# Performance work log

Measured on AMD Instinct MI355X. Metric: run time of the kernel, lower is better.

The kernel has to match this reference:

```python
import jax, jax.numpy as jnp
import numpy as np

B, P, F = 128, 4096, 32
K, D = 8, 64
ITERS = 2
EPS_ATTN = 1e-8
EPS_LN = 1e-5
SCALE = D ** -0.5


def _layernorm(x, g, b):
    mu = jnp.mean(x, axis=-1, keepdims=True)
    var = jnp.mean((x - mu) ** 2, axis=-1, keepdims=True)
    return (x - mu) * jax.lax.rsqrt(var + EPS_LN) * g + b


def setup_inputs() -> dict:
    key = jax.random.key(0)
    ks = jax.random.split(key, 16)
    s = lambda fan_in: 1.0 / np.sqrt(fan_in)
    inp = {
        "x": jax.random.normal(ks[0], (B, P, F), dtype=jnp.float32),
        "noise": jax.random.normal(ks[1], (B, K, D), dtype=jnp.float32),
        "slots_mu": jax.random.normal(ks[2], (1, 1, D), dtype=jnp.float32),
        "slots_sigma": jnp.ones((1, 1, D), dtype=jnp.float32) * 0.1,
        # torch Linear weights: [out, in]
        "Wq": jax.random.uniform(ks[3], (D, D), jnp.float32, -s(D), s(D)),
        "Wk": jax.random.uniform(ks[4], (D, F), jnp.float32, -s(F), s(F)),
        "Wv": jax.random.uniform(ks[5], (D, F), jnp.float32, -s(F), s(F)),
        # GRUCell params: weight_ih/[3D,D], weight_hh/[3D,D], biases [3D]
        "W_ih": jax.random.uniform(ks[6], (3 * D, D), jnp.float32, -s(D), s(D)),
        "W_hh": jax.random.uniform(ks[7], (3 * D, D), jnp.float32, -s(D), s(D)),
        "b_ih": jax.random.uniform(ks[8], (3 * D,), jnp.float32, -s(D), s(D)),
        "b_hh": jax.random.uniform(ks[9], (3 * D,), jnp.float32, -s(D), s(D)),
        "ln_in_g": jnp.ones((F,), jnp.float32),
        "ln_in_b": jnp.zeros((F,), jnp.float32),
        "ln_slots_g": jnp.ones((D,), jnp.float32),
        "ln_slots_b": jnp.zeros((D,), jnp.float32),
        "ff_ln_g": jnp.ones((D,), jnp.float32),
        "ff_ln_b": jnp.zeros((D,), jnp.float32),
        "ff_W1": jax.random.uniform(ks[10], (2 * D, D), jnp.float32, -s(D), s(D)),
        "ff_b1": jax.random.uniform(ks[11], (2 * D,), jnp.float32, -s(D), s(D)),
        "ff_W2": jax.random.uniform(ks[12], (D, 2 * D), jnp.float32, -s(2 * D), s(2 * D)),
        "ff_b2": jax.random.uniform(ks[13], (D,), jnp.float32, -s(2 * D), s(2 * D)),
    }
    return inp


def _gru_cell(x, h, W_ih, W_hh, b_ih, b_hh):
    # x, h: [N, D]
    gi = x @ W_ih.T + b_ih  # [N, 3D]
    gh = h @ W_hh.T + b_hh
    i_r, i_z, i_n = jnp.split(gi, 3, axis=-1)
    h_r, h_z, h_n = jnp.split(gh, 3, axis=-1)
    r = jax.nn.sigmoid(i_r + h_r)
    z = jax.nn.sigmoid(i_z + h_z)
    n = jnp.tanh(i_n + r * h_n)
    return (1.0 - z) * n + z * h


def reference(x, noise, slots_mu, slots_sigma, Wq, Wk, Wv, W_ih, W_hh, b_ih, b_hh,
              ln_in_g, ln_in_b, ln_slots_g, ln_slots_b,
              ff_ln_g, ff_ln_b, ff_W1, ff_b1, ff_W2, ff_b2):
    x_norm = _layernorm(x, ln_in_g, ln_in_b)          # [B,P,F]
    k = x_norm @ Wk.T                                  # [B,P,D]
    v = x_norm @ Wv.T                                  # [B,P,D]
    slots = slots_mu + jnp.abs(slots_sigma) * noise    # [B,K,D]
    last_attn = None
    for _ in range(ITERS):
        slots_prev = slots
        q = _layernorm(slots, ln_slots_g, ln_slots_b) @ Wq.T  # [B,K,D]
        dots = jnp.einsum('bkd,bpd->bkp', q, k) * SCALE       # [B,K,P]
        attn = jax.nn.softmax(dots, axis=1) + EPS_ATTN        # softmax over slots
        attn = attn / jnp.sum(attn, axis=-1, keepdims=True)   # normalize over pixels
        last_attn = attn
        updates = jnp.einsum('bkp,bpd->bkd', attn, v)         # [B,K,D]
        h = _gru_cell(updates.reshape(-1, D), slots_prev.reshape(-1, D),
                      W_ih, W_hh, b_ih, b_hh).reshape(x.shape[0], K, D)
        ff_in = _layernorm(h, ff_ln_g, ff_ln_b)
        ff_out = jax.nn.relu(ff_in @ ff_W1.T + ff_b1) @ ff_W2.T + ff_b2
        slots = h + ff_out
    return slots, last_attn
```

## Files before the change

kernel.cpp:

```cpp
#include <hip/hip_runtime.h>
#include <hip/hip_bf16.h>
#include <stdint.h>

#define Bb 128
#define Pp 4096
#define Ff 32
#define Kk 8
#define Dd 64
#define ROUNDS 2
#define NSLICE 32

constexpr float EPS_ATTN_ = 1e-8f;
constexpr float EPS_LN_   = 1e-5f;
constexpr float SCALE_    = 0.125f;

typedef __attribute__((ext_vector_type(8))) short short8;
typedef __attribute__((ext_vector_type(4))) float floatx4;

__device__ __forceinline__ unsigned short f2bf(float f) {
  union { float f; unsigned u; } c; c.f = f;
  unsigned u = c.u + 0x7fffu + ((c.u >> 16) & 1u);
  return (unsigned short)(u >> 16);
}
__device__ __forceinline__ float bf2f(unsigned h) {
  union { float f; unsigned u; } c; c.u = h << 16;
  return c.f;
}
__device__ __forceinline__ unsigned pkbf(float a, float b) {
  __hip_bfloat162 h2 = __float22bfloat162_rn(make_float2(a, b));
  union { __hip_bfloat162 h; unsigned u; } c; c.h = h2;
  return c.u;
}
__device__ __forceinline__ float wsum(float v) {
  v += __shfl_xor(v, 1, 64);  v += __shfl_xor(v, 2, 64);
  v += __shfl_xor(v, 4, 64);  v += __shfl_xor(v, 8, 64);
  v += __shfl_xor(v, 16, 64); v += __shfl_xor(v, 32, 64);
  return v;
}

template <bool ITER2>
__global__ __launch_bounds__(256, 4) void fattn_kernel(
    const float* __restrict__ x, const unsigned short* __restrict__ qt_bf,
    const float* __restrict__ lg, const float* __restrict__ lb,
    const float* __restrict__ noise, const float* __restrict__ smu,
    const float* __restrict__ ssig, const float* __restrict__ Wq,
    const float* __restrict__ Wk, const float* __restrict__ lsg,
    const float* __restrict__ lsb,
    float* __restrict__ acc_tp, float* __restrict__ Ssp,
    unsigned short* __restrict__ attn_bf) {
  const int b    = blockIdx.x;
  const int yb   = blockIdx.y;
  const int w    = threadIdx.x >> 6;
  const int lane = threadIdx.x & 63;
  const int m    = lane & 15;
  const int quad = lane >> 4;
  const int c    = (lane & 7) * 4;
  __shared__ __align__(16) char smem[40960];
  unsigned short* xb  = (unsigned short*)smem;
  unsigned short* xbT = (unsigned short*)(smem + 20480);
  unsigned short (*A_lds)[8][64] = (unsigned short (*)[8][64])(smem + 36864);

  const float4* xg4 =
      (const float4*)x + ((size_t)b * Pp + (size_t)yb * (ROUNDS * 256)) * 8;
  float4 st[8];
  #pragma unroll
  for (int i = 0; i < 8; ++i)
    st[i] = xg4[w * 512 + i * 64 + lane];

  const float4 lgv = *(const float4*)&lg[c];
  const float4 lbv = *(const float4*)&lb[c];

  short8 aq;
  if (!ITER2) {
    float* wq  = (float*)smem;
    float* wk  = (float*)(smem + 16640);
    float* lnv = (float*)(smem + 25088);
    unsigned short* qtb = (unsigned short*)(smem + 27136);
    {
      const float4* g4 = (const float4*)Wq;
      #pragma unroll
      for (int i = 0; i < 4; ++i) {
        int f4i = threadIdx.x + i * 256;
        float4 v = g4[f4i];
        int fi = f4i * 4, row = fi >> 6, col = fi & 63;
        float* dst = &wq[row * 65 + col];
        dst[0] = v.x; dst[1] = v.y; dst[2] = v.z; dst[3] = v.w;
      }
      const float4* gk = (const float4*)Wk;
      #pragma unroll
      for (int i = 0; i < 2; ++i) {
        int f4i = threadIdx.x + i * 256;
        float4 v = gk[f4i];
        int fi = f4i * 4, row = fi >> 5, col = fi & 31;
        float* dst = &wk[row * 33 + col];
        dst[0] = v.x; dst[1] = v.y; dst[2] = v.z; dst[3] = v.w;
      }
    }
    const int j = lane;
    #pragma unroll
    for (int kk0 = 0; kk0 < 2; ++kk0) {
      const int kk = w + kk0 * 4;
      float s0 = smu[j] + fabsf(ssig[j]) * noise[((size_t)b * Kk + kk) * Dd + j];
      float mu  = wsum(s0) * (1.f / 64.f);
      float dc  = s0 - mu;
      float var = wsum(dc * dc) * (1.f / 64.f);
      lnv[kk * 64 + j] = dc * rsqrtf(var + EPS_LN_) * lsg[j] + lsb[j];
    }
    __syncthreads();
    float qa = 0.f, qb = 0.f;
    #pragma unroll 8
    for (int d = 0; d < Dd; ++d) {
      float wv = wq[j * 65 + d];
      qa = fmaf(wv, lnv[w * 64 + d],       qa);
      qb = fmaf(wv, lnv[(w + 4) * 64 + d], qb);
    }
    __syncthreads();
    lnv[w * 64 + j]       = qa * SCALE_;
    lnv[(w + 4) * 64 + j] = qb * SCALE_;
    __syncthreads();
    {
      const int kq = threadIdx.x >> 5, fq = threadIdx.x & 31;
      float qt = 0.f;
      #pragma unroll 8
      for (int d = 0; d < Dd; ++d) qt = fmaf(lnv[kq * 64 + d], wk[d * 33 + fq], qt);
      qtb[kq * 32 + fq]       = f2bf(qt);
      qtb[(kq + 8) * 32 + fq] = 0;
    }
    __syncthreads();
    aq = *(const short8*)&qtb[m * 32 + quad * 8];
    __syncthreads();
  } else {
    aq = *(const short8*)(qt_bf + ((size_t)b * 16 + m) * Ff + quad * 8);
  }

  float Ss0 = 0.f, Ss1 = 0.f, Ss2 = 0.f, Ss3 = 0.f;
  floatx4 Cg0 = {0.f,0.f,0.f,0.f}, Cg1 = {0.f,0.f,0.f,0.f};

  #pragma unroll 1
  for (int rr = 0; rr < ROUNDS; ++rr) {
    #pragma unroll
    for (int i = 0; i < 8; ++i) {
      float4 v = st[i];
      if (rr + 1 < ROUNDS)
        st[i] = xg4[(rr + 1) * 2048 + w * 512 + i * 64 + lane];
      float s = (v.x + v.y) + (v.z + v.w);
      s += __shfl_xor(s, 1, 64);
      s += __shfl_xor(s, 2, 64);
      s += __shfl_xor(s, 4, 64);
      const float mu = s * (1.f / 32.f);
      const float d0 = v.x - mu, d1 = v.y - mu, d2 = v.z - mu, d3 = v.w - mu;
      float q = fmaf(d0, d0, fmaf(d1, d1, fmaf(d2, d2, d3 * d3)));
      q += __shfl_xor(q, 1, 64);
      q += __shfl_xor(q, 2, 64);
      q += __shfl_xor(q, 4, 64);
      const float rn = rsqrtf(q * (1.f / 32.f) + EPS_LN_);
      const float o0 = fmaf(d0 * rn, lgv.x, lbv.x);
      const float o1 = fmaf(d1 * rn, lgv.y, lbv.y);
      const float o2 = fmaf(d2 * rn, lgv.z, lbv.z);
      const float o3 = fmaf(d3 * rn, lgv.w, lbv.w);
      const unsigned u0 = pkbf(o0, o1), u1 = pkbf(o2, o3);
      const int pxl = w * 64 + i * 8 + (lane >> 3);
      *(uint2*)&xb[pxl * 40 + c] = make_uint2(u0, u1);
      xbT[(c + 0) * 256 + (pxl ^ (((c + 0) & 7) << 3))] = (unsigned short)(u0 & 0xffffu);
      xbT[(c + 1) * 256 + (pxl ^ (((c + 1) & 7) << 3))] = (unsigned short)(u0 >> 16);
      xbT[(c + 2) * 256 + (pxl ^ (((c + 2) & 7) << 3))] = (unsigned short)(u1 & 0xffffu);
      xbT[(c + 3) * 256 + (pxl ^ (((c + 3) & 7) << 3))] = (unsigned short)(u1 >> 16);
    }

    const int p0 = yb * (ROUNDS * 256) + rr * 256;
    #pragma unroll
    for (int t = 0; t < 4; ++t) {
      const int lpx = w * 64 + t * 16 + m;
      const short8 bx = *(const short8*)&xb[lpx * 40 + quad * 8];
      floatx4 C = {0.f, 0.f, 0.f, 0.f};
      C = __builtin_amdgcn_mfma_f32_16x16x32_bf16(aq, bx, C, 0, 0, 0);
      float mx = fmaxf(fmaxf(C[0], C[1]), fmaxf(C[2], C[3]));
      mx = fmaxf(mx, __shfl_xor(mx, 16, 64));
      float e0 = __expf(C[0] - mx), e1 = __expf(C[1] - mx),
            e2 = __expf(C[2] - mx), e3 = __expf(C[3] - mx);
      float s = e0 + e1 + e2 + e3;
      s += __shfl_xor(s, 16, 64);
      float inv = 1.f / s;
      float a0 = fmaf(e0, inv, EPS_ATTN_), a1 = fmaf(e1, inv, EPS_ATTN_);
      float a2 = fmaf(e2, inv, EPS_ATTN_), a3 = fmaf(e3, inv, EPS_ATTN_);
      Ss0 += a0; Ss1 += a1; Ss2 += a2; Ss3 += a3;
      if (quad < 2) {
        const int r0 = quad * 4;
        unsigned c01 = pkbf(a0, a1), c23 = pkbf(a2, a3);
        A_lds[w][r0 + 0][t * 16 + m] = (unsigned short)(c01 & 0xffffu);
        A_lds[w][r0 + 1][t * 16 + m] = (unsigned short)(c01 >> 16);
        A_lds[w][r0 + 2][t * 16 + m] = (unsigned short)(c23 & 0xffffu);
        A_lds[w][r0 + 3][t * 16 + m] = (unsigned short)(c23 >> 16);
      }
    }
    #pragma unroll
    for (int ks = 0; ks < 2; ++ks) {
      const short8 af = *(const short8*)(&A_lds[w][m & 7][ks * 32 + quad * 8]);
      const int pxo = (w * 64 + ks * 32 + quad * 8) ^ ((m & 7) << 3);
      const short8 xg0 = *(const short8*)&xbT[(m)      * 256 + pxo];
      const short8 xg1 = *(const short8*)&xbT[(16 + m) * 256 + pxo];
      Cg0 = __builtin_amdgcn_mfma_f32_16x16x32_bf16(af, xg0, Cg0, 0, 0, 0);
      Cg1 = __builtin_amdgcn_mfma_f32_16x16x32_bf16(af, xg1, Cg1, 0, 0, 0);
    }
    if (ITER2) {
      const int sl = lane >> 3, p8 = (lane & 7) * 8;
      const short8 av = *(const short8*)&A_lds[w][sl][p8];
      *(short8*)(attn_bf + ((size_t)b * Kk + sl) * Pp + p0 + w * 64 + p8) = av;
    }
  }
  Ss0 += __shfl_xor(Ss0,1,64); Ss0 += __shfl_xor(Ss0,2,64); Ss0 += __shfl_xor(Ss0,4,64); Ss0 += __shfl_xor(Ss0,8,64);
  Ss1 += __shfl_xor(Ss1,1,64); Ss1 += __shfl_xor(Ss1,2,64); Ss1 += __shfl_xor(Ss1,4,64); Ss1 += __shfl_xor(Ss1,8,64);
  Ss2 += __shfl_xor(Ss2,1,64); Ss2 += __shfl_xor(Ss2,2,64); Ss2 += __shfl_xor(Ss2,4,64); Ss2 += __shfl_xor(Ss2,8,64);
  Ss3 += __shfl_xor(Ss3,1,64); Ss3 += __shfl_xor(Ss3,2,64); Ss3 += __shfl_xor(Ss3,4,64); Ss3 += __shfl_xor(Ss3,8,64);
  if (quad < 2) {
    const int row = quad * 4;
    const int slice = yb * 4 + w;
    float* tp = acc_tp + (size_t)b * (NSLICE * 256) + (size_t)slice * 256 +
                (size_t)row * 32 + m;
    #pragma unroll
    for (int r = 0; r < 4; ++r) {
      tp[r * 32]      = Cg0[r];
      tp[r * 32 + 16] = Cg1[r];
    }
    if (m == 0) {
      float* sp = Ssp + ((size_t)b * NSLICE + slice) * 8 + row;
      sp[0] = Ss0; sp[1] = Ss1; sp[2] = Ss2; sp[3] = Ss3;
    }
  }
}

__device__ __forceinline__ void stage_gate_pair(
    float* A, float* Bd, const float* Wih, const float* Whh, int g) {
  const float4* gi = (const float4*)Wih + (size_t)g * 1024;
  const float4* gh = (const float4*)Whh + (size_t)g * 1024;
  #pragma unroll
  for (int i = 0; i < 4; ++i) {
    int f4i = threadIdx.x + i * 256;
    float4 vi = gi[f4i], vh = gh[f4i];
    int fi = f4i * 4, row = fi >> 6, col = fi & 63;
    float* da = &A[row * 65 + col];
    float* db = &Bd[row * 65 + col];
    da[0]=vi.x; da[1]=vi.y; da[2]=vi.z; da[3]=vi.w;
    db[0]=vh.x; db[1]=vh.y; db[2]=vh.z; db[3]=vh.w;
  }
}

template <bool LAST>
__device__ void gru_phase(
    char* smem,
    const float* __restrict__ acc_tp, const float* __restrict__ Ssp,
    float* __restrict__ slots,
    const float* __restrict__ noise, const float* __restrict__ smu,
    const float* __restrict__ ssig,
    const float* __restrict__ W_ih, const float* __restrict__ W_hh,
    const float* __restrict__ b_ih, const float* __restrict__ b_hh,
    const float* __restrict__ fg, const float* __restrict__ fb,
    const float* __restrict__ W1, const float* __restrict__ b1,
    const float* __restrict__ W2, const float* __restrict__ b2,
    const float* __restrict__ lsg, const float* __restrict__ lsb,
    const float* __restrict__ Wq, const float* __restrict__ Wv,
    const float* __restrict__ Wk,
    unsigned short* __restrict__ qt_bf, float* __restrict__ out_slots) {
  const int b  = blockIdx.x;
  const int kh = blockIdx.y;
  const int k  = threadIdx.x >> 6;
  const int j  = threadIdx.x & 63;
  const int kg = kh * 4 + k;
  const size_t rk = (size_t)b * Kk + kg;
  float* WS0 = (float*)smem;
  float* At  = (float*)(smem + 16640);
  float* WS1 = (float*)(smem + 16640);
  float* qs  = (float*)(smem + 16640);
  float* WKs = (float*)(smem + 17664);
  float* Ub  = (float*)(smem + 33280);
  float* Hb  = (float*)(smem + 34304);
  float* Tb  = (float*)(smem + 35328);

  {
    const float4* gv = (const float4*)Wv;
    #pragma unroll
    for (int i = 0; i < 2; ++i) {
      int f4i = threadIdx.x + i * 256;
      float4 v = gv[f4i];
      int fi = f4i * 4, row = fi >> 5, col = fi & 31;
      float* d_ = &WS0[row * 33 + col];
      d_[0]=v.x; d_[1]=v.y; d_[2]=v.z; d_[3]=v.w;
    }
  }
  float S = 0.f;
  #pragma unroll
  for (int y2 = 0; y2 < NSLICE; ++y2) S += Ssp[((size_t)b * NSLICE + y2) * 8 + kg];
  if (j < Ff) {
    const float* tp = acc_tp + (size_t)b * (NSLICE * 256) + (size_t)kg * 32 + j;
    float t = 0.f;
    #pragma unroll
    for (int y2 = 0; y2 < NSLICE; ++y2) t += tp[y2 * 256];
    At[k * Ff + j] = t;
  }
  float h;
  if (LAST) h = slots[rk * Dd + j];
  else      h = smu[j] + fabsf(ssig[j]) * noise[rk * Dd + j];
  Hb[k * Dd + j] = h;
  __syncthreads();
  float u = 0.f;
  #pragma unroll 8
  for (int f = 0; f < Ff; ++f) u = fmaf(WS0[j * 33 + f], At[k * Ff + f], u);
  u /= S;
  Ub[k * Dd + j] = u;
  __syncthreads();

  float gr, hr, gz, hz, gn, hn_;
  stage_gate_pair(WS0, WS1, W_ih, W_hh, 0);
  __syncthreads();
  gr = b_ih[j]; hr = b_hh[j];
  #pragma unroll 4
  for (int d = 0; d < Dd; ++d) {
    gr = fmaf(WS0[j * 65 + d], Ub[k * Dd + d], gr);
    hr = fmaf(WS1[j * 65 + d], Hb[k * Dd + d], hr);
  }
  __syncthreads();
  stage_gate_pair(WS0, WS1, W_ih, W_hh, 1);
  __syncthreads();
  gz = b_ih[64 + j]; hz = b_hh[64 + j];
  #pragma unroll 4
  for (int d = 0; d < Dd; ++d) {
    gz = fmaf(WS0[j * 65 + d], Ub[k * Dd + d], gz);
    hz = fmaf(WS1[j * 65 + d], Hb[k * Dd + d], hz);
  }
  __syncthreads();
  stage_gate_pair(WS0, WS1, W_ih, W_hh, 2);
  __syncthreads();
  gn = b_ih[128 + j]; hn_ = b_hh[128 + j];
  #pragma unroll 4
  for (int d = 0; d < Dd; ++d) {
    gn  = fmaf(WS0[j * 65 + d], Ub[k * Dd + d], gn);
    hn_ = fmaf(WS1[j * 65 + d], Hb[k * Dd + d], hn_);
  }
  const float r = 1.f / (1.f + __expf(-(gr + hr)));
  const float z = 1.f / (1.f + __expf(-(gz + hz)));
  const float n = tanhf(fmaf(r, hn_, gn));
  const float hnew = fmaf(z, h - n, n);
  float mu  = wsum(hnew) * (1.f / 64.f);
  float dc  = hnew - mu;
  float var = wsum(dc * dc) * (1.f / 64.f);
  float fi_ = dc * rsqrtf(var + EPS_LN_) * fg[j] + fb[j];
  __syncthreads();
  Ub[k * Dd + j] = fi_;
  {
    const float4* g1 = (const float4*)W1;
    #pragma unroll
    for (int i = 0; i < 8; ++i) {
      int f4i = threadIdx.x + i * 256;
      float4 v = g1[f4i];
      int fi = f4i * 4, row = fi >> 6, col = fi & 63;
      float* d_ = &WS0[row * 65 + col];
      d_[0]=v.x; d_[1]=v.y; d_[2]=v.z; d_[3]=v.w;
    }
  }
  __syncthreads();
  float f1a = b1[j], f1b = b1[64 + j];
  #pragma unroll 4
  for (int d = 0; d < Dd; ++d) {
    const float t = Ub[k * Dd + d];
    f1a = fmaf(WS0[j * 65 + d],        t, f1a);
    f1b = fmaf(WS0[(64 + j) * 65 + d], t, f1b);
  }
  f1a = fmaxf(f1a, 0.f);
  f1b = fmaxf(f1b, 0.f);
  Tb[k * 128 + j]      = f1a;
  Tb[k * 128 + 64 + j] = f1b;
  __syncthreads();
  {
    const float4* g2 = (const float4*)W2;
    #pragma unroll
    for (int i = 0; i < 8; ++i) {
      int f4i = threadIdx.x + i * 256;
      float4 v = g2[f4i];
      int fi = f4i * 4, row = fi >> 7, col = fi & 127;
      float* d_ = &WS0[row * 129 + col];
      d_[0]=v.x; d_[1]=v.y; d_[2]=v.z; d_[3]=v.w;
    }
  }
  __syncthreads();
  float o = b2[j];
  #pragma unroll 4
  for (int e = 0; e < 2 * Dd; ++e) o = fmaf(WS0[j * 129 + e], Tb[k * 128 + e], o);
  const float sn = hnew + o;
  if (!LAST) {
    slots[rk * Dd + j] = sn;
    float mq = wsum(sn) * (1.f / 64.f);
    float dq = sn - mq;
    float vq = wsum(dq * dq) * (1.f / 64.f);
    float xq = dq * rsqrtf(vq + EPS_LN_) * lsg[j] + lsb[j];
    __syncthreads();
    Ub[k * Dd + j] = xq;
    {
      const float4* gq = (const float4*)Wq;
      #pragma unroll
      for (int i = 0; i < 4; ++i) {
        int f4i = threadIdx.x + i * 256;
        float4 v = gq[f4i];
        int fi = f4i * 4, row = fi >> 6, col = fi & 63;
        float* d_ = &WS0[row * 65 + col];
        d_[0]=v.x; d_[1]=v.y; d_[2]=v.z; d_[3]=v.w;
      }
      const float4* gk2 = (const float4*)Wk;
      #pragma unroll
      for (int i = 0; i < 2; ++i) {
        int f4i = threadIdx.x + i * 256;
        float4 v = gk2[f4i];
        int fi = f4i * 4, row = fi >> 5, col = fi & 31;
        float* d_ = &WKs[row * 33 + col];
        d_[0]=v.x; d_[1]=v.y; d_[2]=v.z; d_[3]=v.w;
      }
    }
    __syncthreads();
    float q = 0.f;
    #pragma unroll 8
    for (int d = 0; d < Dd; ++d) q = fmaf(WS0[j * 65 + d], Ub[k * Dd + d], q);
    qs[k * Dd + j] = q * SCALE_;
    __syncthreads();
    if (j < Ff) {
      float qt = 0.f;
      #pragma unroll 8
      for (int d = 0; d < Dd; ++d) qt = fmaf(qs[k * Dd + d], WKs[d * 33 + j], qt);
      qt_bf[((size_t)b * 16 + kg) * Ff + j]     = f2bf(qt);
      qt_bf[((size_t)b * 16 + kg + 8) * Ff + j] = 0;
    }
  } else {
    out_slots[rk * Dd + j] = sn;
  }
}

__global__ __launch_bounds__(256) void gru1_kernel(
    const float* __restrict__ acc_tp, const float* __restrict__ Ssp,
    float* __restrict__ slots,
    const float* __restrict__ noise, const float* __restrict__ smu,
    const float* __restrict__ ssig,
    const float* __restrict__ W_ih, const float* __restrict__ W_hh,
    const float* __restrict__ b_ih, const float* __restrict__ b_hh,
    const float* __restrict__ fg, const float* __restrict__ fb,
    const float* __restrict__ W1, const float* __restrict__ b1,
    const float* __restrict__ W2, const float* __restrict__ b2,
    const float* __restrict__ lsg, const float* __restrict__ lsb,
    const float* __restrict__ Wq, const float* __restrict__ Wv,
    const float* __restrict__ Wk, unsigned short* __restrict__ qt_bf) {
  __shared__ __align__(16) char smem[37376];
  gru_phase<false>(smem, acc_tp, Ssp, slots, noise, smu, ssig, W_ih, W_hh,
                   b_ih, b_hh, fg, fb, W1, b1, W2, b2, lsg, lsb, Wq, Wv, Wk,
                   qt_bf, nullptr);
}

__global__ __launch_bounds__(256) void gru2_scale_kernel(
    const float* __restrict__ acc_tp, const float* __restrict__ Ssp,
    float* __restrict__ slots,
    const float* __restrict__ noise, const float* __restrict__ smu,
    const float* __restrict__ ssig,
    const float* __restrict__ W_ih, const float* __restrict__ W_hh,
    const float* __restrict__ b_ih, const float* __restrict__ b_hh,
    const float* __restrict__ fg, const float* __restrict__ fb,
    const float* __restrict__ W1, const float* __restrict__ b1,
    const float* __restrict__ W2, const float* __restrict__ b2,
    const float* __restrict__ lsg, const float* __restrict__ lsb,
    const float* __restrict__ Wq, const float* __restrict__ Wv,
    const float* __restrict__ Wk,
    const unsigned short* __restrict__ attn_bf,
    float* __restrict__ out_slots, float* __restrict__ out_attn) {
  __shared__ __align__(16) char smem[37376];
  if (blockIdx.y < 2) {
    gru_phase<true>(smem, acc_tp, Ssp, slots, noise, smu, ssig, W_ih, W_hh,
                    b_ih, b_hh, fg, fb, W1, b1, W2, b2, lsg, lsb, Wq, Wv, Wk,
                    nullptr, out_slots);
  } else {
    const int b = blockIdx.x;
    const int s = blockIdx.y - 2;
    float* Sbuf = (float*)smem;
    if (threadIdx.x < 8) {
      float S = 0.f;
      #pragma unroll
      for (int y2 = 0; y2 < NSLICE; ++y2)
        S += Ssp[((size_t)b * NSLICE + y2) * 8 + threadIdx.x];
      Sbuf[threadIdx.x] = 1.f / S;
    }
    __syncthreads();
    #pragma unroll
    for (int i = 0; i < 2; ++i) {
      int g = threadIdx.x + i * 256;
      int slot = g >> 6;
      int px4 = (g & 63) * 4;
      size_t off = ((size_t)b * Kk + slot) * Pp + (size_t)s * 256 + px4;
      uint2 v = *(const uint2*)(attn_bf + off);
      float inv = Sbuf[slot];
      float4 ov;
      ov.x = bf2f(v.x & 0xffffu) * inv;
      ov.y = bf2f(v.x >> 16)     * inv;
      ov.z = bf2f(v.y & 0xffffu) * inv;
      ov.w = bf2f(v.y >> 16)     * inv;
      *(float4*)(out_attn + off) = ov;
    }
  }
}

extern "C" void kernel_launch(void* const* d_in, const int* in_sizes, int n_in,
                              void* d_out, int out_size, void* d_ws, size_t ws_size,
                              hipStream_t stream) {
  const float* x      = (const float*)d_in[0];
  const float* noise  = (const float*)d_in[1];
  const float* smu    = (const float*)d_in[2];
  const float* ssig   = (const float*)d_in[3];
  const float* Wq     = (const float*)d_in[4];
  const float* Wk     = (const float*)d_in[5];
  const float* Wv     = (const float*)d_in[6];
  const float* W_ih   = (const float*)d_in[7];
  const float* W_hh   = (const float*)d_in[8];
  const float* b_ih   = (const float*)d_in[9];
  const float* b_hh   = (const float*)d_in[10];
  const float* ln_in_g = (const float*)d_in[11];
  const float* ln_in_b = (const float*)d_in[12];
  const float* ln_s_g  = (const float*)d_in[13];
  const float* ln_s_b  = (const float*)d_in[14];
  const float* ff_g   = (const float*)d_in[15];
  const float* ff_b   = (const float*)d_in[16];
  const float* W1     = (const float*)d_in[17];
  const float* b1     = (const float*)d_in[18];
  const float* W2     = (const float*)d_in[19];
  const float* b2     = (const float*)d_in[20];

  char* ws = (char*)d_ws;
  unsigned short* qt_bf = (unsigned short*)(ws);
  float* slots   = (float*)(ws + 131072);
  float* acc_tp  = (float*)(ws + 393216);
  float* Ssp     = (float*)(ws + 4587520);
  unsigned short* attn_bf = (unsigned short*)(ws + 4718592);

  float* out_slots = (float*)d_out;
  float* out_attn  = out_slots + (size_t)Bb * Kk * Dd;

  fattn_kernel<false><<<dim3(Bb, 8), dim3(256), 0, stream>>>(
      x, nullptr, ln_in_g, ln_in_b, noise, smu, ssig, Wq, Wk, ln_s_g, ln_s_b,
      acc_tp, Ssp, nullptr);
  gru1_kernel<<<dim3(Bb, 2), dim3(256), 0, stream>>>(
      acc_tp, Ssp, slots, noise, smu, ssig, W_ih, W_hh, b_ih, b_hh, ff_g, ff_b,
      W1, b1, W2, b2, ln_s_g, ln_s_b, Wq, Wv, Wk, qt_bf);
  fattn_kernel<true><<<dim3(Bb, 8), dim3(256), 0, stream>>>(
      x, qt_bf, ln_in_g, ln_in_b, nullptr, nullptr, nullptr, nullptr, nullptr,
      nullptr, nullptr, acc_tp, Ssp, attn_bf);
  gru2_scale_kernel<<<dim3(Bb, 18), dim3(256), 0, stream>>>(
      acc_tp, Ssp, slots, noise, smu, ssig, W_ih, W_hh, b_ih, b_hh, ff_g, ff_b,
      W1, b1, W2, b2, ln_s_g, ln_s_b, Wq, Wv, Wk, attn_bf, out_slots, out_attn);
}
```

Baseline: 206.7 us.

## Cache layer-normalized bf16 inputs for second attention pass and swizzle attention LDS

The first attention kernel now writes the layer-normalized input, packed as bf16, to a workspace buffer. The second-iteration kernel reads that buffer instead of re-reading the fp32 input and recomputing layernorm, which halves its input traffic and removes the shuffle reductions. The first pass gains an extra 32 MB of global writes in exchange. Separately, the attention-weight LDS tile is XOR-swizzled by slot row to reduce bank conflicts on its stores and reads.

Measured after the change: 215.3 us. 1.04x slower.

```diff
diff --git a/kernel.cpp b/kernel.cpp
--- a/kernel.cpp
+++ b/kernel.cpp
@@ -47,7 +47,7 @@
     const float* __restrict__ Wk, const float* __restrict__ lsg,
     const float* __restrict__ lsb,
     float* __restrict__ acc_tp, float* __restrict__ Ssp,
-    unsigned short* __restrict__ attn_bf) {
+    unsigned short* __restrict__ attn_bf, unsigned short* __restrict__ xn) {
   const int b    = blockIdx.x;
   const int yb   = blockIdx.y;
   const int w    = threadIdx.x >> 6;
@@ -62,13 +62,25 @@
 
   const float4* xg4 =
       (const float4*)x + ((size_t)b * Pp + (size_t)yb * (ROUNDS * 256)) * 8;
+  unsigned short* xnb =
+      xn + ((size_t)b * Pp + (size_t)yb * (ROUNDS * 256)) * 32;
   float4 st[8];
-  #pragma unroll
-  for (int i = 0; i < 8; ++i)
-    st[i] = xg4[w * 512 + i * 64 + lane];
-
-  const float4 lgv = *(const float4*)&lg[c];
-  const float4 lbv = *(const float4*)&lb[c];
+  uint2  st2[8];
+  if (!ITER2) {
+    #pragma unroll
+    for (int i = 0; i < 8; ++i)
+      st[i] = xg4[w * 512 + i * 64 + lane];
+  } else {
+    #pragma unroll
+    for (int i = 0; i < 8; ++i)
+      st2[i] = *(const uint2*)&xnb[(size_t)(w * 64 + i * 8 + (lane >> 3)) * 32 + c];
+  }
+
+  float4 lgv, lbv;
+  if (!ITER2) {
+    lgv = *(const float4*)&lg[c];
+    lbv = *(const float4*)&lb[c];
+  }
 
   short8 aq;
   if (!ITER2) {
@@ -140,26 +152,35 @@
   for (int rr = 0; rr < ROUNDS; ++rr) {
     #pragma unroll
     for (int i = 0; i < 8; ++i) {
-      float4 v = st[i];
-      if (rr + 1 < ROUNDS)
-        st[i] = xg4[(rr + 1) * 2048 + w * 512 + i * 64 + lane];
-      float s = (v.x + v.y) + (v.z + v.w);
-      s += __shfl_xor(s, 1, 64);
-      s += __shfl_xor(s, 2, 64);
-      s += __shfl_xor(s, 4, 64);
-      const float mu = s * (1.f / 32.f);
-      const float d0 = v.x - mu, d1 = v.y - mu, d2 = v.z - mu, d3 = v.w - mu;
-      float q = fmaf(d0, d0, fmaf(d1, d1, fmaf(d2, d2, d3 * d3)));
-      q += __shfl_xor(q, 1, 64);
-      q += __shfl_xor(q, 2, 64);
-      q += __shfl_xor(q, 4, 64);
-      const float rn = rsqrtf(q * (1.f / 32.f) + EPS_LN_);
-      const float o0 = fmaf(d0 * rn, lgv.x, lbv.x);
-      const float o1 = fmaf(d1 * rn, lgv.y, lbv.y);
-      const float o2 = fmaf(d2 * rn, lgv.z, lbv.z);
-      const float o3 = fmaf(d3 * rn, lgv.w, lbv.w);
-      const unsigned u0 = pkbf(o0, o1), u1 = pkbf(o2, o3);
       const int pxl = w * 64 + i * 8 + (lane >> 3);
+      unsigned u0, u1;
+      if (!ITER2) {
+        float4 v = st[i];
+        if (rr + 1 < ROUNDS)
+          st[i] = xg4[(rr + 1) * 2048 + w * 512 + i * 64 + lane];
+        float s = (v.x + v.y) + (v.z + v.w);
+        s += __shfl_xor(s, 1, 64);
+        s += __shfl_xor(s, 2, 64);
+        s += __shfl_xor(s, 4, 64);
+        const float mu = s * (1.f / 32.f);
+        const float d0 = v.x - mu, d1 = v.y - mu, d2 = v.z - mu, d3 = v.w - mu;
+        float q = fmaf(d0, d0, fmaf(d1, d1, fmaf(d2, d2, d3 * d3)));
+        q += __shfl_xor(q, 1, 64);
+        q += __shfl_xor(q, 2, 64);
+        q += __shfl_xor(q, 4, 64);
+        const float rn = rsqrtf(q * (1.f / 32.f) + EPS_LN_);
+        const float o0 = fmaf(d0 * rn, lgv.x, lbv.x);
+        const float o1 = fmaf(d1 * rn, lgv.y, lbv.y);
+        const float o2 = fmaf(d2 * rn, lgv.z, lbv.z);
+        const float o3 = fmaf(d3 * rn, lgv.w, lbv.w);
+        u0 = pkbf(o0, o1); u1 = pkbf(o2, o3);
+        *(uint2*)&xnb[(size_t)(rr * 256 + pxl) * 32 + c] = make_uint2(u0, u1);
+      } else {
+        uint2 uv = st2[i];
+        if (rr + 1 < ROUNDS)
+          st2[i] = *(const uint2*)&xnb[(size_t)((rr + 1) * 256 + pxl) * 32 + c];
+        u0 = uv.x; u1 = uv.y;
+      }
       *(uint2*)&xb[pxl * 40 + c] = make_uint2(u0, u1);
       xbT[(c + 0) * 256 + (pxl ^ (((c + 0) & 7) << 3))] = (unsigned short)(u0 & 0xffffu);
       xbT[(c + 1) * 256 + (pxl ^ (((c + 1) & 7) << 3))] = (unsigned short)(u0 >> 16);
@@ -187,15 +208,17 @@
       if (quad < 2) {
         const int r0 = quad * 4;
         unsigned c01 = pkbf(a0, a1), c23 = pkbf(a2, a3);
-        A_lds[w][r0 + 0][t * 16 + m] = (unsigned short)(c01 & 0xffffu);
-        A_lds[w][r0 + 1][t * 16 + m] = (unsigned short)(c01 >> 16);
-        A_lds[w][r0 + 2][t * 16 + m] = (unsigned short)(c23 & 0xffffu);
-        A_lds[w][r0 + 3][t * 16 + m] = (unsigned short)(c23 >> 16);
+        const int col = t * 16 + m;
+        A_lds[w][r0 + 0][col ^ ((r0 + 0) << 3)] = (unsigned short)(c01 & 0xffffu);
+        A_lds[w][r0 + 1][col ^ ((r0 + 1) << 3)] = (unsigned short)(c01 >> 16);
+        A_lds[w][r0 + 2][col ^ ((r0 + 2) << 3)] = (unsigned short)(c23 & 0xffffu);
+        A_lds[w][r0 + 3][col ^ ((r0 + 3) << 3)] = (unsigned short)(c23 >> 16);
       }
     }
     #pragma unroll
     for (int ks = 0; ks < 2; ++ks) {
-      const short8 af = *(const short8*)(&A_lds[w][m & 7][ks * 32 + quad * 8]);
+      const int acol = (ks * 32 + quad * 8) ^ ((m & 7) << 3);
+      const short8 af = *(const short8*)(&A_lds[w][m & 7][acol]);
       const int pxo = (w * 64 + ks * 32 + quad * 8) ^ ((m & 7) << 3);
       const short8 xg0 = *(const short8*)&xbT[(m)      * 256 + pxo];
       const short8 xg1 = *(const short8*)&xbT[(16 + m) * 256 + pxo];
@@ -204,7 +227,7 @@
     }
     if (ITER2) {
       const int sl = lane >> 3, p8 = (lane & 7) * 8;
-      const short8 av = *(const short8*)&A_lds[w][sl][p8];
+      const short8 av = *(const short8*)&A_lds[w][sl][p8 ^ (sl << 3)];
       *(short8*)(attn_bf + ((size_t)b * Kk + sl) * Pp + p0 + w * 64 + p8) = av;
     }
   }
@@ -532,19 +555,20 @@
   float* acc_tp  = (float*)(ws + 393216);
   float* Ssp     = (float*)(ws + 4587520);
   unsigned short* attn_bf = (unsigned short*)(ws + 4718592);
+  unsigned short* xn      = (unsigned short*)(ws + 13107200);
 
   float* out_slots = (float*)d_out;
   float* out_attn  = out_slots + (size_t)Bb * Kk * Dd;
 
   fattn_kernel<false><<<dim3(Bb, 8), dim3(256), 0, stream>>>(
       x, nullptr, ln_in_g, ln_in_b, noise, smu, ssig, Wq, Wk, ln_s_g, ln_s_b,
-      acc_tp, Ssp, nullptr);
+      acc_tp, Ssp, nullptr, xn);
   gru1_kernel<<<dim3(Bb, 2), dim3(256), 0, stream>>>(
       acc_tp, Ssp, slots, noise, smu, ssig, W_ih, W_hh, b_ih, b_hh, ff_g, ff_b,
       W1, b1, W2, b2, ln_s_g, ln_s_b, Wq, Wv, Wk, qt_bf);
   fattn_kernel<true><<<dim3(Bb, 8), dim3(256), 0, stream>>>(
       x, qt_bf, ln_in_g, ln_in_b, nullptr, nullptr, nullptr, nullptr, nullptr,
-      nullptr, nullptr, acc_tp, Ssp, attn_bf);
+      nullptr, nullptr, acc_tp, Ssp, attn_bf, xn);
   gru2_scale_kernel<<<dim3(Bb, 18), dim3(256), 0, stream>>>(
       acc_tp, Ssp, slots, noise, smu, ssig, W_ih, W_hh, b_ih, b_hh, ff_g, ff_b,
       W1, b1, W2, b2, ln_s_g, ln_s_b, Wq, Wv, Wk, attn_bf, out_slots, out_attn);
```
